# Optimization experiments

Hardware: AMD Instinct MI355X
Metric: run time of the kernel (lower is better)

The kernel has to match this reference:

```python
import jax, jax.numpy as jnp
import numpy as np

HIDDEN = 512
BATCH = 32
SEQ = 4096


def setup_inputs() -> dict:
    key = jax.random.key(0)
    ks = jax.random.split(key, 8)
    s = 1.0 / np.sqrt(HIDDEN)
    return {
        "encoder_outputs": jax.random.normal(ks[0], (BATCH, SEQ, HIDDEN), jnp.float32),
        "decoder_hidden": jax.random.normal(ks[1], (BATCH, HIDDEN), jnp.float32),
        "W_enc": jax.random.uniform(ks[2], (HIDDEN, HIDDEN), jnp.float32, -s, s),
        "b_enc": jax.random.uniform(ks[3], (HIDDEN,), jnp.float32, -s, s),
        "W_dec": jax.random.uniform(ks[4], (HIDDEN, HIDDEN), jnp.float32, -s, s),
        "b_dec": jax.random.uniform(ks[5], (HIDDEN,), jnp.float32, -s, s),
        "W_v": jax.random.uniform(ks[6], (HIDDEN, 1), jnp.float32, -s, s),
        "b_v": jax.random.uniform(ks[7], (1,), jnp.float32, -s, s),
    }


def reference(encoder_outputs, decoder_hidden, W_enc, b_enc, W_dec, b_dec, W_v, b_v):
    # (b, s, h) projected encoder states
    enc_proj = jnp.einsum("bsh,hk->bsk", encoder_outputs, W_enc) + b_enc
    # (b, 1, h) projected decoder state, broadcast-added over seq
    dec_proj = (decoder_hidden @ W_dec + b_dec)[:, None, :]
    # score: (b, s, 1)
    score = jnp.tanh(enc_proj + dec_proj) @ W_v + b_v
    attention_weights = jax.nn.softmax(score, axis=1)  # softmax over seq_len
    # context: (b, h) weighted sum of encoder outputs
    context = jnp.sum(attention_weights * encoder_outputs, axis=1)
    return context, jnp.squeeze(attention_weights, -1)
```

## Files before the change

### kernel.cpp

```cpp
#include <hip/hip_runtime.h>
#include <hip/hip_bf16.h>

typedef __attribute__((ext_vector_type(8))) short bf16x8;
typedef __attribute__((ext_vector_type(4))) float f32x4;

#define HID 512
#define NB 32
#define SEQL 4096
#define BM 64
#define BK 32
#define NKC 16
#define NBLK 2048

#define WS_BP    0
#define WS_DPROJ (512*1024)
#define WS_SUM   (576*1024)

__device__ __forceinline__ short f2bf(float f) {
    unsigned u = __float_as_uint(f);
    unsigned r = (u + 0x7fffu + ((u >> 16) & 1u)) >> 16;
    return (short)r;
}

__device__ __forceinline__ float fast_tanh(float x) {
    float e = __expf(2.0f * x);
    float r = __builtin_amdgcn_rcpf(e + 1.0f);
    return 1.0f - 2.0f * r;
}

__device__ __forceinline__ void async16(const void* g, void* l) {
    __builtin_amdgcn_global_load_lds((__attribute__((address_space(1))) void*)(g),
                                     (__attribute__((address_space(3))) void*)(l),
                                     16, 0, 0);
}

__global__ void k_pre(const float* __restrict__ We, short* __restrict__ Bp,
                      const float* __restrict__ dec, const float* __restrict__ Wd,
                      const float* __restrict__ be, const float* __restrict__ bd,
                      float* __restrict__ dproj, float* __restrict__ out,
                      float* __restrict__ sumacc) {
    const int blk = blockIdx.x, t = threadIdx.x;
    if (blk < 128) {
        int tid  = blk * 256 + t;
        int lane = tid & 63;
        int nt   = (tid >> 6) & 31;
        int kc   = tid >> 11;
        int k0   = kc * 32 + (lane >> 4) * 8;
        int n    = nt * 16 + (lane & 15);
        bf16x8 v;
#pragma unroll
        for (int j = 0; j < 8; ++j) v[j] = f2bf(We[(size_t)(k0 + j) * HID + n]);
        *(bf16x8*)&Bp[(size_t)tid * 8] = v;
    } else if (blk < 640) {
        __shared__ float red[8][33];
        int bid2 = blk - 128;
        int b  = bid2 >> 4, kg = bid2 & 15;
        int kl = t & 31,    hc = t >> 5;
        int k  = kg * 32 + kl;
        const float* dr = dec + (size_t)b * HID;
        float a = 0.f;
#pragma unroll 8
        for (int j = 0; j < 64; ++j) {
            int h = hc * 64 + j;
            a += dr[h] * Wd[(size_t)h * HID + k];
        }
        red[hc][kl] = a;
        __syncthreads();
        if (hc == 0) {
            float s = be[k] + bd[k];
#pragma unroll
            for (int c = 0; c < 8; ++c) s += red[c][kl];
            dproj[(size_t)b * HID + k] = s;
        }
    } else {
        int bz = blk - 640;
        out[bz * 256 + t] = 0.f;
        if (bz == 0 && t < NB) sumacc[t] = 0.f;
    }
}

__global__ __launch_bounds__(256, 2)
void k_main(const float* __restrict__ E, const short* __restrict__ Bp,
            const float* __restrict__ dproj, const float* __restrict__ Wv,
            float* __restrict__ out, float* __restrict__ sumacc) {
    __shared__ short As[2][BM][BK + 8];
    __shared__ short Bs[2][BK * HID];
    __shared__ float fbuf[640];
    __shared__ float pbuf[BM];

    const int tid  = threadIdx.x;
    const int wave = tid >> 6, lane = tid & 63;
    const int quad = lane >> 4, l15 = lane & 15;
    const int bid  = blockIdx.x;
    const int row0 = bid * BM;
    const int b    = bid >> 6;

    f32x4 acc[4][8];
#pragma unroll
    for (int r = 0; r < 4; ++r)
#pragma unroll
        for (int c = 0; c < 8; ++c) acc[r][c] = (f32x4){0.f, 0.f, 0.f, 0.f};

    const int arow = tid >> 2, akq = tid & 3;
    const float* aptr = E + (size_t)(row0 + arow) * HID + akq * 8;

    float4 pa0[2], pa1[2];

    pa0[0] = *(const float4*)(aptr);
    pa1[0] = *(const float4*)(aptr + 4);
    pa0[1] = *(const float4*)(aptr + 32);
    pa1[1] = *(const float4*)(aptr + 36);
    {
        const short* bsrc = Bp;
#pragma unroll
        for (int i = 0; i < 8; ++i) {
            int off = (i * 4 + wave) * 512;
            async16(bsrc + off + lane * 8, &Bs[0][off]);
        }
        bf16x8 av;
        av[0] = f2bf(pa0[0].x); av[1] = f2bf(pa0[0].y); av[2] = f2bf(pa0[0].z); av[3] = f2bf(pa0[0].w);
        av[4] = f2bf(pa1[0].x); av[5] = f2bf(pa1[0].y); av[6] = f2bf(pa1[0].z); av[7] = f2bf(pa1[0].w);
        *(bf16x8*)&As[0][arow][akq * 8] = av;
    }

#pragma unroll
    for (int kc = 0; kc < NKC; ++kc) {
        const int cur = kc & 1, nxt = cur ^ 1;
        __syncthreads();

        {
            const int src = (kc + 2 < NKC) ? (kc + 2) : 0;
            pa0[kc & 1] = *(const float4*)(aptr + src * 32);
            pa1[kc & 1] = *(const float4*)(aptr + src * 32 + 4);
        }
        if (kc + 1 < NKC) {
            const short* bsrc = Bp + (size_t)(kc + 1) * 16384;
#pragma unroll
            for (int i = 0; i < 8; ++i) {
                int off = (i * 4 + wave) * 512;
                async16(bsrc + off + lane * 8, &Bs[nxt][off]);
            }
        }

        bf16x8 fa[4];
#pragma unroll
        for (int r = 0; r < 4; ++r) fa[r] = *(bf16x8*)&As[cur][r * 16 + l15][quad * 8];
#pragma unroll
        for (int c = 0; c < 8; ++c) {
            int nt = wave * 8 + c;
            bf16x8 fb = *(bf16x8*)&Bs[cur][(nt * 64 + lane) * 8];
#pragma unroll
            for (int r = 0; r < 4; ++r)
                acc[r][c] = __builtin_amdgcn_mfma_f32_16x16x32_bf16(fa[r], fb, acc[r][c], 0, 0, 0);
        }

        if (kc + 1 < NKC) {
            float4 a0 = pa0[nxt], a1 = pa1[nxt];
            bf16x8 av;
            av[0] = f2bf(a0.x); av[1] = f2bf(a0.y); av[2] = f2bf(a0.z); av[3] = f2bf(a0.w);
            av[4] = f2bf(a1.x); av[5] = f2bf(a1.y); av[6] = f2bf(a1.z); av[7] = f2bf(a1.w);
            *(bf16x8*)&As[nxt][arow][akq * 8] = av;
        }
    }

    float part[4][4];
#pragma unroll
    for (int r = 0; r < 4; ++r)
#pragma unroll
        for (int g = 0; g < 4; ++g) part[r][g] = 0.f;
    const float* dp = dproj + (size_t)b * HID;
#pragma unroll
    for (int c = 0; c < 8; ++c) {
        int col = wave * 128 + c * 16 + l15;
        float dv = dp[col];
        float wv = Wv[col];
#pragma unroll
        for (int r = 0; r < 4; ++r)
#pragma unroll
            for (int g = 0; g < 4; ++g)
                part[r][g] += fast_tanh(acc[r][c][g] + dv) * wv;
    }
#pragma unroll
    for (int r = 0; r < 4; ++r)
#pragma unroll
        for (int g = 0; g < 4; ++g) {
            float v = part[r][g];
            v += __shfl_xor(v, 1); v += __shfl_xor(v, 2);
            v += __shfl_xor(v, 4); v += __shfl_xor(v, 8);
            part[r][g] = v;
        }
    if (l15 == 0) {
#pragma unroll
        for (int r = 0; r < 4; ++r)
#pragma unroll
            for (int g = 0; g < 4; ++g)
                fbuf[wave * 64 + r * 16 + quad * 4 + g] = part[r][g];
    }
    __syncthreads();
    if (tid < 64) {
        float s  = fbuf[tid] + fbuf[64 + tid] + fbuf[128 + tid] + fbuf[192 + tid];
        float pv = __expf(s);
        pbuf[tid] = pv;
        out[(size_t)NB * HID + row0 + tid] = pv;
        float t2 = pv;
        t2 += __shfl_xor(t2, 1);  t2 += __shfl_xor(t2, 2);  t2 += __shfl_xor(t2, 4);
        t2 += __shfl_xor(t2, 8);  t2 += __shfl_xor(t2, 16); t2 += __shfl_xor(t2, 32);
        if (tid == 0) atomicAdd(&sumacc[b], t2);
    }
    __syncthreads();

    const int hq = tid & 127, rh = tid >> 7;
    const float4* E4 = (const float4*)E;
    size_t cbase = (size_t)(row0 + rh * 32) * (HID / 4) + hq;
    float4 ca = {0.f, 0.f, 0.f, 0.f};
#pragma unroll 4
    for (int rr = 0; rr < 32; ++rr) {
        float w  = pbuf[rh * 32 + rr];
        float4 e = E4[cbase + (size_t)rr * (HID / 4)];
        ca.x += w * e.x; ca.y += w * e.y; ca.z += w * e.z; ca.w += w * e.w;
    }
    if (rh == 1) {
        fbuf[hq] = ca.x; fbuf[128 + hq] = ca.y; fbuf[256 + hq] = ca.z; fbuf[384 + hq] = ca.w;
    }
    __syncthreads();
    if (rh == 0) {
        ca.x += fbuf[hq]; ca.y += fbuf[128 + hq]; ca.z += fbuf[256 + hq]; ca.w += fbuf[384 + hq];
        float* cg = out + (size_t)b * HID + hq * 4;
        atomicAdd(cg + 0, ca.x); atomicAdd(cg + 1, ca.y);
        atomicAdd(cg + 2, ca.z); atomicAdd(cg + 3, ca.w);
    }
}

__global__ void k_finish(float* __restrict__ out, const float* __restrict__ sumacc) {
    int b = blockIdx.x, t = threadIdx.x;
    float rs = 1.0f / sumacc[b];
    for (int i = t; i < HID; i += 256)
        out[(size_t)b * HID + i] *= rs;
    float* ow = out + (size_t)NB * HID + (size_t)b * SEQL;
    for (int i = t; i < SEQL; i += 256)
        ow[i] *= rs;
}

extern "C" void kernel_launch(void* const* d_in, const int* in_sizes, int n_in,
                              void* d_out, int out_size, void* d_ws, size_t ws_size,
                              hipStream_t stream) {
    const float* E   = (const float*)d_in[0];
    const float* dec = (const float*)d_in[1];
    const float* We  = (const float*)d_in[2];
    const float* be  = (const float*)d_in[3];
    const float* Wd  = (const float*)d_in[4];
    const float* bd  = (const float*)d_in[5];
    const float* Wv  = (const float*)d_in[6];
    float* out = (float*)d_out;
    char*  ws  = (char*)d_ws;
    short* Bp     = (short*)(ws + WS_BP);
    float* dproj  = (float*)(ws + WS_DPROJ);
    float* sumacc = (float*)(ws + WS_SUM);

    k_pre<<<704, 256, 0, stream>>>(We, Bp, dec, Wd, be, bd, dproj, out, sumacc);
    k_main<<<NBLK, 256, 0, stream>>>(E, Bp, dproj, Wv, out, sumacc);
    k_finish<<<NB, 256, 0, stream>>>(out, sumacc);
}
```

Before: 478.3 us.

## Stage full A tile in LDS upfront and stream B fragments from global into registers

The K-loop no longer double-buffers A and B through LDS. The whole 64x512 encoder tile is loaded once and converted to bf16 into a padded LDS buffer. B fragments are read directly from global memory into registers with one-step prefetch, which removes the per-iteration __syncthreads and the async LDS copies of B. The cost is a larger up-front load phase with no overlap, more register pressure from the prefetched fragments, and B traffic that now goes through L2/L1 separately for each block instead of through shared LDS.

Result: slower. 492.5 us (+3.0%).

```diff
diff --git a/kernel.cpp b/kernel.cpp
--- a/kernel.cpp
+++ b/kernel.cpp
@@ -8,9 +8,10 @@
 #define NB 32
 #define SEQL 4096
 #define BM 64
-#define BK 32
 #define NKC 16
 #define NBLK 2048
+#define APAD 8
+#define AW (HID + APAD)
 
 #define WS_BP    0
 #define WS_DPROJ (512*1024)
@@ -26,12 +27,6 @@
     float e = __expf(2.0f * x);
     float r = __builtin_amdgcn_rcpf(e + 1.0f);
     return 1.0f - 2.0f * r;
-}
-
-__device__ __forceinline__ void async16(const void* g, void* l) {
-    __builtin_amdgcn_global_load_lds((__attribute__((address_space(1))) void*)(g),
-                                     (__attribute__((address_space(3))) void*)(l),
-                                     16, 0, 0);
 }
 
 __global__ void k_pre(const float* __restrict__ We, short* __restrict__ Bp,
@@ -83,8 +78,7 @@
 void k_main(const float* __restrict__ E, const short* __restrict__ Bp,
             const float* __restrict__ dproj, const float* __restrict__ Wv,
             float* __restrict__ out, float* __restrict__ sumacc) {
-    __shared__ short As[2][BM][BK + 8];
-    __shared__ short Bs[2][BK * HID];
+    __shared__ short As[BM][AW];
     __shared__ float fbuf[640];
     __shared__ float pbuf[BM];
 
@@ -101,66 +95,55 @@
 #pragma unroll
         for (int c = 0; c < 8; ++c) acc[r][c] = (f32x4){0.f, 0.f, 0.f, 0.f};
 
-    const int arow = tid >> 2, akq = tid & 3;
-    const float* aptr = E + (size_t)(row0 + arow) * HID + akq * 8;
-
-    float4 pa0[2], pa1[2];
-
-    pa0[0] = *(const float4*)(aptr);
-    pa1[0] = *(const float4*)(aptr + 4);
-    pa0[1] = *(const float4*)(aptr + 32);
-    pa1[1] = *(const float4*)(aptr + 36);
-    {
-        const short* bsrc = Bp;
-#pragma unroll
-        for (int i = 0; i < 8; ++i) {
-            int off = (i * 4 + wave) * 512;
-            async16(bsrc + off + lane * 8, &Bs[0][off]);
-        }
-        bf16x8 av;
-        av[0] = f2bf(pa0[0].x); av[1] = f2bf(pa0[0].y); av[2] = f2bf(pa0[0].z); av[3] = f2bf(pa0[0].w);
-        av[4] = f2bf(pa1[0].x); av[5] = f2bf(pa1[0].y); av[6] = f2bf(pa1[0].z); av[7] = f2bf(pa1[0].w);
-        *(bf16x8*)&As[0][arow][akq * 8] = av;
-    }
+    const float4* E4 = (const float4*)E + (size_t)row0 * (HID / 4);
+    const int drow = tid >> 7;
+    const int dcol = (tid & 127) * 4;
+#pragma unroll
+    for (int ph = 0; ph < 4; ++ph) {
+        float4 v[8];
+#pragma unroll
+        for (int j = 0; j < 8; ++j)
+            v[j] = E4[(size_t)(ph * 8 + j) * 256 + tid];
+#pragma unroll
+        for (int j = 0; j < 8; ++j) {
+            int row = (ph * 8 + j) * 2 + drow;
+            short4 s;
+            s.x = f2bf(v[j].x); s.y = f2bf(v[j].y);
+            s.z = f2bf(v[j].z); s.w = f2bf(v[j].w);
+            *(short4*)&As[row][dcol] = s;
+        }
+    }
+
+    const short* bbase = Bp + ((size_t)(wave * 8) * 64 + lane) * 8;
+    bf16x8 fb[2][4][2];
+    bf16x8 fbr[2][8];
+#pragma unroll
+    for (int c = 0; c < 8; ++c)
+        fbr[0][c] = *(const bf16x8*)(bbase + (size_t)c * 64 * 8);
+
+    __syncthreads();
+
+    bf16x8 fa[2][4];
+#pragma unroll
+    for (int r = 0; r < 4; ++r)
+        fa[0][r] = *(const bf16x8*)&As[r * 16 + l15][quad * 8];
 
 #pragma unroll
     for (int kc = 0; kc < NKC; ++kc) {
         const int cur = kc & 1, nxt = cur ^ 1;
-        __syncthreads();
-
-        {
-            const int src = (kc + 2 < NKC) ? (kc + 2) : 0;
-            pa0[kc & 1] = *(const float4*)(aptr + src * 32);
-            pa1[kc & 1] = *(const float4*)(aptr + src * 32 + 4);
-        }
         if (kc + 1 < NKC) {
-            const short* bsrc = Bp + (size_t)(kc + 1) * 16384;
-#pragma unroll
-            for (int i = 0; i < 8; ++i) {
-                int off = (i * 4 + wave) * 512;
-                async16(bsrc + off + lane * 8, &Bs[nxt][off]);
-            }
-        }
-
-        bf16x8 fa[4];
-#pragma unroll
-        for (int r = 0; r < 4; ++r) fa[r] = *(bf16x8*)&As[cur][r * 16 + l15][quad * 8];
-#pragma unroll
-        for (int c = 0; c < 8; ++c) {
-            int nt = wave * 8 + c;
-            bf16x8 fb = *(bf16x8*)&Bs[cur][(nt * 64 + lane) * 8];
+#pragma unroll
+            for (int c = 0; c < 8; ++c)
+                fbr[nxt][c] = *(const bf16x8*)(bbase + ((size_t)(kc + 1) * 2048 + c * 64) * 8);
 #pragma unroll
             for (int r = 0; r < 4; ++r)
-                acc[r][c] = __builtin_amdgcn_mfma_f32_16x16x32_bf16(fa[r], fb, acc[r][c], 0, 0, 0);
-        }
-
-        if (kc + 1 < NKC) {
-            float4 a0 = pa0[nxt], a1 = pa1[nxt];
-            bf16x8 av;
-            av[0] = f2bf(a0.x); av[1] = f2bf(a0.y); av[2] = f2bf(a0.z); av[3] = f2bf(a0.w);
-            av[4] = f2bf(a1.x); av[5] = f2bf(a1.y); av[6] = f2bf(a1.z); av[7] = f2bf(a1.w);
-            *(bf16x8*)&As[nxt][arow][akq * 8] = av;
-        }
+                fa[nxt][r] = *(const bf16x8*)&As[r * 16 + l15][(kc + 1) * 32 + quad * 8];
+        }
+#pragma unroll
+        for (int c = 0; c < 8; ++c)
+#pragma unroll
+            for (int r = 0; r < 4; ++r)
+                acc[r][c] = __builtin_amdgcn_mfma_f32_16x16x32_bf16(fa[cur][r], fbr[cur][c], acc[r][c], 0, 0, 0);
     }
 
     float part[4][4];
@@ -210,13 +193,13 @@
     __syncthreads();
 
     const int hq = tid & 127, rh = tid >> 7;
-    const float4* E4 = (const float4*)E;
+    const float4* Eb = (const float4*)E;
     size_t cbase = (size_t)(row0 + rh * 32) * (HID / 4) + hq;
     float4 ca = {0.f, 0.f, 0.f, 0.f};
 #pragma unroll 4
     for (int rr = 0; rr < 32; ++rr) {
         float w  = pbuf[rh * 32 + rr];
-        float4 e = E4[cbase + (size_t)rr * (HID / 4)];
+        float4 e = Eb[cbase + (size_t)rr * (HID / 4)];
         ca.x += w * e.x; ca.y += w * e.y; ca.z += w * e.z; ca.w += w * e.w;
     }
     if (rh == 1) {
```

## Replace double-buffered K-loop pipeline with single-buffered load-sync-compute loop

Applied to the files above, without the earlier changes.

Removes the double-buffered LDS staging and register prefetch of the encoder tile and weight chunks, and uses single LDS buffers with a barrier before and after each K-chunk's MFMA work. This halves LDS footprint and register use for prefetch, which could allow more resident blocks. In exchange, global-load latency is no longer overlapped with matrix math, and an extra barrier is added per iteration.

Result: faster. 449.2 us (-6.1%).

```diff
diff --git a/kernel.cpp b/kernel.cpp
--- a/kernel.cpp
+++ b/kernel.cpp
@@ -83,8 +83,8 @@
 void k_main(const float* __restrict__ E, const short* __restrict__ Bp,
             const float* __restrict__ dproj, const float* __restrict__ Wv,
             float* __restrict__ out, float* __restrict__ sumacc) {
-    __shared__ short As[2][BM][BK + 8];
-    __shared__ short Bs[2][BK * HID];
+    __shared__ short As[BM][BK + 8];
+    __shared__ short Bs[BK * HID];
     __shared__ float fbuf[640];
     __shared__ float pbuf[BM];
 
@@ -104,63 +104,32 @@
     const int arow = tid >> 2, akq = tid & 3;
     const float* aptr = E + (size_t)(row0 + arow) * HID + akq * 8;
 
-    float4 pa0[2], pa1[2];
-
-    pa0[0] = *(const float4*)(aptr);
-    pa1[0] = *(const float4*)(aptr + 4);
-    pa0[1] = *(const float4*)(aptr + 32);
-    pa1[1] = *(const float4*)(aptr + 36);
-    {
-        const short* bsrc = Bp;
+    for (int kc = 0; kc < NKC; ++kc) {
+        float4 a0 = *(const float4*)(aptr + kc * 32);
+        float4 a1 = *(const float4*)(aptr + kc * 32 + 4);
+        bf16x8 av;
+        av[0] = f2bf(a0.x); av[1] = f2bf(a0.y); av[2] = f2bf(a0.z); av[3] = f2bf(a0.w);
+        av[4] = f2bf(a1.x); av[5] = f2bf(a1.y); av[6] = f2bf(a1.z); av[7] = f2bf(a1.w);
+        *(bf16x8*)&As[arow][akq * 8] = av;
+        const short* bsrc = Bp + (size_t)kc * 16384;
 #pragma unroll
         for (int i = 0; i < 8; ++i) {
             int off = (i * 4 + wave) * 512;
-            async16(bsrc + off + lane * 8, &Bs[0][off]);
-        }
-        bf16x8 av;
-        av[0] = f2bf(pa0[0].x); av[1] = f2bf(pa0[0].y); av[2] = f2bf(pa0[0].z); av[3] = f2bf(pa0[0].w);
-        av[4] = f2bf(pa1[0].x); av[5] = f2bf(pa1[0].y); av[6] = f2bf(pa1[0].z); av[7] = f2bf(pa1[0].w);
-        *(bf16x8*)&As[0][arow][akq * 8] = av;
-    }
-
-#pragma unroll
-    for (int kc = 0; kc < NKC; ++kc) {
-        const int cur = kc & 1, nxt = cur ^ 1;
+            async16(bsrc + off + lane * 8, &Bs[off]);
+        }
         __syncthreads();
-
-        {
-            const int src = (kc + 2 < NKC) ? (kc + 2) : 0;
-            pa0[kc & 1] = *(const float4*)(aptr + src * 32);
-            pa1[kc & 1] = *(const float4*)(aptr + src * 32 + 4);
-        }
-        if (kc + 1 < NKC) {
-            const short* bsrc = Bp + (size_t)(kc + 1) * 16384;
-#pragma unroll
-            for (int i = 0; i < 8; ++i) {
-                int off = (i * 4 + wave) * 512;
-                async16(bsrc + off + lane * 8, &Bs[nxt][off]);
-            }
-        }
-
         bf16x8 fa[4];
 #pragma unroll
-        for (int r = 0; r < 4; ++r) fa[r] = *(bf16x8*)&As[cur][r * 16 + l15][quad * 8];
+        for (int r = 0; r < 4; ++r) fa[r] = *(bf16x8*)&As[r * 16 + l15][quad * 8];
 #pragma unroll
         for (int c = 0; c < 8; ++c) {
             int nt = wave * 8 + c;
-            bf16x8 fb = *(bf16x8*)&Bs[cur][(nt * 64 + lane) * 8];
+            bf16x8 fb = *(bf16x8*)&Bs[(nt * 64 + lane) * 8];
 #pragma unroll
             for (int r = 0; r < 4; ++r)
                 acc[r][c] = __builtin_amdgcn_mfma_f32_16x16x32_bf16(fa[r], fb, acc[r][c], 0, 0, 0);
         }
-
-        if (kc + 1 < NKC) {
-            float4 a0 = pa0[nxt], a1 = pa1[nxt];
-            bf16x8 av;
-            av[0] = f2bf(a0.x); av[1] = f2bf(a0.y); av[2] = f2bf(a0.z); av[3] = f2bf(a0.w);
-            av[4] = f2bf(a1.x); av[5] = f2bf(a1.y); av[6] = f2bf(a1.z); av[7] = f2bf(a1.w);
-            *(bf16x8*)&As[nxt][arow][akq * 8] = av;
-        }
+        __syncthreads();
     }
 
     float part[4][4];
```
